# Kernel tuning notes

Measured on AMD Instinct MI355X. Metric: run time of the kernel, lower is better.

## Reference

```python
import jax, jax.numpy as jnp
import numpy as np

N_NODES = 100000


def gcn_conv(x, edge_index, W, b, n):
    """PyG-style GCNConv: h = D^-1/2 (A + I) D^-1/2 (x W) + b."""
    h = x @ W  # [n, out]
    loops = jnp.arange(n, dtype=edge_index.dtype)
    src = jnp.concatenate([edge_index[0], loops])
    dst = jnp.concatenate([edge_index[1], loops])
    deg = jax.ops.segment_sum(jnp.ones_like(dst, dtype=h.dtype), dst, num_segments=n)
    dinv = jnp.where(deg > 0, jax.lax.rsqrt(deg), 0.0)
    norm = dinv[src] * dinv[dst]  # [E+n]
    msg = h[src] * norm[:, None]
    out = jax.ops.segment_sum(msg, dst, num_segments=n)
    return out + b


def setup_inputs() -> dict:
    key = jax.random.key(0)
    ks = jax.random.split(key, 12)
    n, f, hid, c, e = N_NODES, 128, 16, 32, 3200000
    x = jax.random.normal(ks[0], (n, f), dtype=jnp.float32)
    edge_index_pos = jax.random.randint(ks[1], (2, e), 0, n, dtype=jnp.int32)
    edge_index_neg = jax.random.randint(ks[2], (2, e), 0, n, dtype=jnp.int32)
    def glorot(k, fi, fo):
        lim = np.sqrt(6.0 / (fi + fo)).astype(np.float32)
        return jax.random.uniform(k, (fi, fo), minval=-lim, maxval=lim, dtype=jnp.float32)
    return {
        "x": x,
        "edge_index_pos": edge_index_pos,
        "edge_index_neg": edge_index_neg,
        "W1p": glorot(ks[3], f, hid), "b1p": jnp.zeros((hid,), jnp.float32),
        "W1n": glorot(ks[4], f, hid), "b1n": jnp.zeros((hid,), jnp.float32),
        "W2p": glorot(ks[5], hid, c), "b2p": jnp.zeros((c,), jnp.float32),
        "W2n": glorot(ks[6], hid, c), "b2n": jnp.zeros((c,), jnp.float32),
    }


def reference(x, edge_index_pos, edge_index_neg, W1p, b1p, W1n, b1n, W2p, b2p, W2n, b2n):
    n = x.shape[0]
    # layer 1: relu(pos) - relu(neg)
    h = (jax.nn.relu(gcn_conv(x, edge_index_pos, W1p, b1p, n))
         - jax.nn.relu(gcn_conv(x, edge_index_neg, W1n, b1n, n)))
    # dropout is identity in eval mode (training=False)
    h = (jax.nn.relu(gcn_conv(h, edge_index_pos, W2p, b2p, n))
         - jax.nn.relu(gcn_conv(h, edge_index_neg, W2n, b2n, n)))
    return jax.nn.log_softmax(h, axis=1)
```

## Files before the change

### kernel.cpp

```cpp
#include <hip/hip_runtime.h>
#include <hip/hip_fp16.h>


#define BSHIFT 8
#define BSZ 256
#define MAX_NBK 512
#define FILL_CAP 13056
#define SORT_CAP 12032

__device__ __forceinline__ int chunk_of_block(int bid, int NCH) {
  return (NCH % 8 == 0) ? (bid % 8) * (NCH / 8) + bid / 8 : bid;
}


__global__ __launch_bounds__(256) void bucket_count2(
    const int* __restrict__ eP, const int* __restrict__ eN,
    int E, int CH, int NCH, int NBK, int* __restrict__ ccP, int* __restrict__ ccN) {
  __shared__ int cnt[MAX_NBK];
  const int* dsts = (blockIdx.y ? eN : eP) + E;
  int* cc = blockIdx.y ? ccN : ccP;
  const int c = chunk_of_block(blockIdx.x, NCH);
  for (int i = threadIdx.x; i < NBK; i += 256) cnt[i] = 0;
  __syncthreads();
  int base = c * CH, end = min(E, base + CH);
  for (int idx = base + threadIdx.x; idx < end; idx += 256)
    atomicAdd(&cnt[dsts[idx] >> BSHIFT], 1);
  __syncthreads();
  for (int i = threadIdx.x; i < NBK; i += 256)
    cc[(size_t)c * NBK + i] = cnt[i];
}

__global__ __launch_bounds__(512) void col_scan2(
    int* __restrict__ ccP, int* __restrict__ ccN, int NCH, int NBK,
    int* __restrict__ totP, int* __restrict__ totN) {
  __shared__ int s[512];
  int* cc = blockIdx.y ? ccN : ccP;
  int* tot = blockIdx.y ? totN : totP;
  int b = blockIdx.x, t = threadIdx.x;
  int v = (t < NCH) ? cc[(size_t)t * NBK + b] : 0;
  s[t] = v;
  for (int off = 1; off < 512; off <<= 1) {
    __syncthreads();
    int a = (t >= off) ? s[t - off] : 0;
    __syncthreads();
    s[t] += a;
  }
  __syncthreads();
  if (t < NCH) cc[(size_t)t * NBK + b] = s[t] - v;
  if (t == 511) tot[b] = s[511];
}

__global__ __launch_bounds__(512) void base_scan(
    const int* __restrict__ totP, const int* __restrict__ totN, int NBK,
    int* __restrict__ baseP, int* __restrict__ baseN,
    int* __restrict__ rowP, int* __restrict__ rowN, int n, int E) {
  __shared__ int sp[512], sn[512];
  __shared__ int carryP, carryN;
  int t = threadIdx.x;
  if (t == 0) { carryP = 0; carryN = 0; }
  __syncthreads();
  for (int tile = 0; tile < NBK; tile += 512) {
    int idx = tile + t;
    int vp = (idx < NBK) ? totP[idx] : 0;
    int vn = (idx < NBK) ? totN[idx] : 0;
    sp[t] = vp; sn[t] = vn;
    for (int off = 1; off < 512; off <<= 1) {
      __syncthreads();
      int ap = (t >= off) ? sp[t - off] : 0;
      int an = (t >= off) ? sn[t - off] : 0;
      __syncthreads();
      sp[t] += ap; sn[t] += an;
    }
    __syncthreads();
    if (idx < NBK) {
      baseP[idx] = carryP + sp[t] - vp;
      baseN[idx] = carryN + sn[t] - vn;
    }
    __syncthreads();
    if (t == 0) { carryP += sp[511]; carryN += sn[511]; }
    __syncthreads();
  }
  if (t == 0) {
    baseP[NBK] = E; baseN[NBK] = E;
    rowP[n] = E; rowN[n] = E;
  }
}

__global__ __launch_bounds__(512) void bucket_fill3(
    const int* __restrict__ eP, const int* __restrict__ eN,
    int E, int CH, int NCH, int NBK,
    const int* __restrict__ ccP, const int* __restrict__ ccN,
    const int* __restrict__ totP, const int* __restrict__ totN,
    const int* __restrict__ basP, const int* __restrict__ basN,
    unsigned* __restrict__ prP, unsigned* __restrict__ prN) {
  __shared__ unsigned obuf[FILL_CAP];
  __shared__ int chofs[MAX_NBK], hist[MAX_NBK], lofs[MAX_NBK], cur[MAX_NBK];
  __shared__ int s[512];
  const int* edges = blockIdx.y ? eN : eP;
  const int* cc = blockIdx.y ? ccN : ccP;
  const int* tot = blockIdx.y ? totN : totP;
  const int* bas = blockIdx.y ? basN : basP;
  unsigned* pairs = blockIdx.y ? prN : prP;
  const int c = chunk_of_block(blockIdx.x, NCH);
  const int t = threadIdx.x;

  int h = 0;
  if (t < NBK) {
    int o0 = cc[(size_t)c * NBK + t];
    int o1 = (c + 1 < NCH) ? cc[(size_t)(c + 1) * NBK + t] : tot[t];
    chofs[t] = o0;
    h = o1 - o0;
    hist[t] = h;
  }
  s[t] = h;
  for (int off = 1; off < 512; off <<= 1) {
    __syncthreads();
    int a = (t >= off) ? s[t - off] : 0;
    __syncthreads();
    s[t] += a;
  }
  __syncthreads();
  if (t < NBK) { lofs[t] = s[t] - hist[t]; cur[t] = s[t] - hist[t]; }
  __syncthreads();

  int base = c * CH, end = min(E, base + CH);
  for (int idx = base + t; idx < end; idx += 512) {
    int sv = edges[idx], d = edges[E + idx];
    int b = d >> BSHIFT;
    int pos = atomicAdd(&cur[b], 1);
    obuf[pos] = (unsigned)sv | ((unsigned)(d & (BSZ - 1)) << 24);
  }
  __syncthreads();

  if (t < NBK) {
    int cnt = hist[t], lo = lofs[t];
    unsigned* dst = pairs + (size_t)bas[t] + chofs[t];
    for (int j = 0; j < cnt; ++j) dst[j] = obuf[lo + j];
  }
}

__global__ __launch_bounds__(256) void tile_sort3(
    const unsigned* __restrict__ prP, const unsigned* __restrict__ prN,
    const int* __restrict__ basP, const int* __restrict__ basN, int n,
    float* __restrict__ dinvP, float* __restrict__ dinvN,
    int* __restrict__ rowP, int* __restrict__ rowN,
    unsigned* __restrict__ srcsP, unsigned* __restrict__ srcsN) {
  __shared__ unsigned obuf[SORT_CAP];
  __shared__ int hist[BSZ];
  __shared__ int scn[BSZ];
  __shared__ int cur[BSZ];
  const unsigned* pairs = blockIdx.y ? prN : prP;
  const int* base = blockIdx.y ? basN : basP;
  float* dinv = blockIdx.y ? dinvN : dinvP;
  int* rowoff = blockIdx.y ? rowN : rowP;
  unsigned* srcs = blockIdx.y ? srcsN : srcsP;
  const int b = blockIdx.x, t = threadIdx.x;
  const int s0 = base[b], s1 = base[b + 1], cnt = s1 - s0;
  hist[t] = 0;
  __syncthreads();
  for (int i = s0 + t; i < s1; i += 256)
    atomicAdd(&hist[pairs[i] >> 24], 1);
  __syncthreads();
  scn[t] = hist[t];
  __syncthreads();
  for (int off = 1; off < BSZ; off <<= 1) {
    int v = (t >= off) ? scn[t - off] : 0;
    __syncthreads();
    scn[t] += v;
    __syncthreads();
  }
  {
    int excl = scn[t] - hist[t];
    cur[t] = excl;
    int node = b * BSZ + t;
    if (node < n) {
      rowoff[node] = s0 + excl;
      dinv[node] = rsqrtf(1.0f + (float)hist[t]);
    }
  }
  __syncthreads();
  if (cnt <= SORT_CAP) {
    for (int i = s0 + t; i < s1; i += 256) {
      unsigned p = pairs[i];
      int pos = atomicAdd(&cur[p >> 24], 1);
      obuf[pos] = p & 0xFFFFFFu;
    }
    __syncthreads();
    for (int i = t; i < cnt; i += 256) srcs[s0 + i] = obuf[i];
  } else {
    for (int i = s0 + t; i < s1; i += 256) {
      unsigned p = pairs[i];
      int pos = atomicAdd(&cur[p >> 24], 1);
      srcs[s0 + pos] = p & 0xFFFFFFu;
    }
  }
}

__global__ __launch_bounds__(256) void xw1_kernel(
    const float* __restrict__ x, const float* __restrict__ Wp, const float* __restrict__ Wn,
    const float* __restrict__ dinvP, const float* __restrict__ dinvN,
    __half* __restrict__ hp, __half* __restrict__ hn, int n)
{
  __shared__ float xs[16 * 132];
  __shared__ float wp[128 * 16], wn[128 * 16];
  const int tid = threadIdx.x;
  const int rowBase = blockIdx.x * 16;

  for (int idx = tid; idx < 512; idx += 256) {
    ((float4*)wp)[idx] = ((const float4*)Wp)[idx];
    ((float4*)wn)[idx] = ((const float4*)Wn)[idx];
  }
  const int nrows = min(16, n - rowBase);
  for (int idx = tid; idx < nrows * 32; idx += 256) {
    int r = idx >> 5, c4 = idx & 31;
    float4 v = ((const float4*)(x + (size_t)(rowBase + r) * 128))[c4];
    *(float4*)(xs + r * 132 + c4 * 4) = v;
  }
  __syncthreads();

  const int r = tid >> 4, c = tid & 15;
  const int i = rowBase + r;
  if (i < n) {
    float ap = 0.f, an = 0.f;
    #pragma unroll
    for (int k = 0; k < 128; ++k) {
      float xv = xs[r * 132 + k];
      ap += xv * wp[k * 16 + c];
      an += xv * wn[k * 16 + c];
    }
    hp[(size_t)i * 16 + c] = __float2half(ap * dinvP[i]);
    hn[(size_t)i * 16 + c] = __float2half(an * dinvN[i]);
  }
}

__device__ __forceinline__ void fma_mix2(float& aLo, float& aHi, unsigned h2, float one) {
  asm("v_fma_mix_f32 %0, %2, %3, %0 op_sel:[0,0,0] op_sel_hi:[1,0,0]\n\t"
      "v_fma_mix_f32 %1, %2, %3, %1 op_sel:[1,0,0] op_sel_hi:[1,0,0]"
      : "+v"(aLo), "+v"(aHi)
      : "v"(h2), "v"(one));
}

__device__ __forceinline__ void seg_sum4(
    const unsigned* __restrict__ srcs, int e, int e1,
    const __half* __restrict__ tab, int lane4, float one,
    float& f0, float& f1, float& f2, float& f3)
{
  float g0 = 0.f, g1 = 0.f, g2 = 0.f, g3 = 0.f;
  for (; e + 8 <= e1; e += 8) {
    unsigned a[8];
    #pragma unroll
    for (int j = 0; j < 8; ++j) a[j] = srcs[e + j];
    uint2 v[8];
    #pragma unroll
    for (int j = 0; j < 8; ++j)
      v[j] = *(const uint2*)(tab + (size_t)a[j] * 16 + lane4 * 4);
    #pragma unroll
    for (int j = 0; j < 8; j += 2) {
      fma_mix2(f0, f1, v[j].x, one);
      fma_mix2(f2, f3, v[j].y, one);
      fma_mix2(g0, g1, v[j + 1].x, one);
      fma_mix2(g2, g3, v[j + 1].y, one);
    }
  }
  for (; e + 2 <= e1; e += 2) {
    unsigned a0 = srcs[e], a1 = srcs[e + 1];
    uint2 v0 = *(const uint2*)(tab + (size_t)a0 * 16 + lane4 * 4);
    uint2 v1 = *(const uint2*)(tab + (size_t)a1 * 16 + lane4 * 4);
    fma_mix2(f0, f1, v0.x, one);
    fma_mix2(f2, f3, v0.y, one);
    fma_mix2(g0, g1, v1.x, one);
    fma_mix2(g2, g3, v1.y, one);
  }
  if (e < e1) {
    uint2 v = *(const uint2*)(tab + (size_t)srcs[e] * 16 + lane4 * 4);
    fma_mix2(f0, f1, v.x, one);
    fma_mix2(f2, f3, v.y, one);
  }
  f0 += g0; f1 += g1; f2 += g2; f3 += g3;
}

__global__ __launch_bounds__(256) void agg_split(
    const unsigned* __restrict__ srcP, const int* __restrict__ rowP,
    const unsigned* __restrict__ srcN, const int* __restrict__ rowN,
    const __half* __restrict__ inP, const __half* __restrict__ inN,
    const float* __restrict__ dinvP, const float* __restrict__ dinvN,
    float* __restrict__ tmpP, float* __restrict__ tmpN, int n)
{
  const int gb = blockIdx.x;
  const int xcd = gb & 7;
  const int sign = xcd >> 2;
  const int nblk = (gb >> 3) * 4 + (xcd & 3);
  const int lane4 = threadIdx.x & 3, grp = threadIdx.x >> 2;
  const int i = nblk * 64 + grp;
  if (i >= n) return;

  const unsigned* srcs = sign ? srcN : srcP;
  const int* row = sign ? rowN : rowP;
  const __half* tab = sign ? inN : inP;
  const float* dinv = sign ? dinvN : dinvP;
  float* tmp = sign ? tmpN : tmpP;

  const float one = 1.0f;
  float f0 = 0.f, f1 = 0.f, f2 = 0.f, f3 = 0.f;
  uint2 self = *(const uint2*)(tab + (size_t)i * 16 + lane4 * 4);
  fma_mix2(f0, f1, self.x, one);
  fma_mix2(f2, f3, self.y, one);
  seg_sum4(srcs, row[i], row[i + 1], tab, lane4, one, f0, f1, f2, f3);
  const float d = dinv[i];
  float4 o;
  o.x = f0 * d; o.y = f1 * d; o.z = f2 * d; o.w = f3 * d;
  *(float4*)(tmp + (size_t)i * 16 + lane4 * 4) = o;
}

__global__ __launch_bounds__(256) void combine1(
    const float* __restrict__ tmpP, const float* __restrict__ tmpN,
    const float* __restrict__ bp, const float* __restrict__ bn,
    const float* __restrict__ dinvP, const float* __restrict__ dinvN,
    __half* __restrict__ Gp, __half* __restrict__ Gn, long long total)
{
  long long j = (long long)blockIdx.x * 256 + threadIdx.x;
  if (j >= total) return;
  int i = (int)(j >> 4), lane = (int)(j & 15);
  float ap = bp[lane] + tmpP[j];
  float an = bn[lane] + tmpN[j];
  float h = fmaxf(ap, 0.f) - fmaxf(an, 0.f);
  Gp[j] = __float2half(h * dinvP[i]);
  Gn[j] = __float2half(h * dinvN[i]);
}

__global__ __launch_bounds__(256) void final2(
    const float* __restrict__ Up, const float* __restrict__ Un,
    const float* __restrict__ W2p, const float* __restrict__ W2n,
    const float* __restrict__ b2p, const float* __restrict__ b2n,
    float* __restrict__ out, int n)
{
  __shared__ float wp[16 * 32], wn[16 * 32];
  for (int i = threadIdx.x; i < 512; i += 256) { wp[i] = W2p[i]; wn[i] = W2n[i]; }
  __syncthreads();

  const int tid = threadIdx.x;
  const int lane = tid & 15, grp = tid >> 4;
  const int i = blockIdx.x * 16 + grp;
  if (i >= n) return;

  float tp = Up[(size_t)i * 16 + lane];
  float tn = Un[(size_t)i * 16 + lane];

  float ap0 = b2p[lane], ap1 = b2p[lane + 16];
  float an0 = b2n[lane], an1 = b2n[lane + 16];
  #pragma unroll
  for (int k = 0; k < 16; ++k) {
    float tpk = __shfl(tp, k, 16);
    float tnk = __shfl(tn, k, 16);
    ap0 += tpk * wp[k * 32 + lane];
    ap1 += tpk * wp[k * 32 + lane + 16];
    an0 += tnk * wn[k * 32 + lane];
    an1 += tnk * wn[k * 32 + lane + 16];
  }
  float v0 = fmaxf(ap0, 0.f) - fmaxf(an0, 0.f);
  float v1 = fmaxf(ap1, 0.f) - fmaxf(an1, 0.f);
  float m = fmaxf(v0, v1);
  #pragma unroll
  for (int off = 8; off > 0; off >>= 1) m = fmaxf(m, __shfl_xor(m, off, 16));
  float s = __expf(v0 - m) + __expf(v1 - m);
  #pragma unroll
  for (int off = 8; off > 0; off >>= 1) s += __shfl_xor(s, off, 16);
  float ls = __logf(s);
  out[(size_t)i * 32 + lane] = v0 - m - ls;
  out[(size_t)i * 32 + lane + 16] = v1 - m - ls;
}

extern "C" void kernel_launch(void* const* d_in, const int* in_sizes, int n_in,
                              void* d_out, int out_size, void* d_ws, size_t ws_size,
                              hipStream_t stream) {
  const float* x   = (const float*)d_in[0];
  const int*   eP  = (const int*)d_in[1];
  const int*   eN  = (const int*)d_in[2];
  const float* W1p = (const float*)d_in[3];
  const float* b1p = (const float*)d_in[4];
  const float* W1n = (const float*)d_in[5];
  const float* b1n = (const float*)d_in[6];
  const float* W2p = (const float*)d_in[7];
  const float* b2p = (const float*)d_in[8];
  const float* W2n = (const float*)d_in[9];
  const float* b2n = (const float*)d_in[10];
  float* out = (float*)d_out;

  const int HID = in_sizes[4];
  const int F   = in_sizes[3] / HID;
  const int n   = in_sizes[0] / F;
  const int E   = in_sizes[1] / 2;
  (void)out_size; (void)n_in; (void)ws_size;

  const int NBK = (n + BSZ - 1) >> BSHIFT;
  const int CH  = (((E + 255) / 256) + 255) & ~255;
  const int NCH = (E + CH - 1) / CH;

  char* p = (char*)d_ws;
  auto alloc = [&](size_t bytes) { char* r = p; p += (bytes + 255) & ~(size_t)255; return r; };

  int*      ccP   = (int*)alloc((size_t)NCH * NBK * 4);
  int*      ccN   = (int*)alloc((size_t)NCH * NBK * 4);
  int*      totP  = (int*)alloc((size_t)NBK * 4);
  int*      totN  = (int*)alloc((size_t)NBK * 4);
  int*      basP  = (int*)alloc((size_t)(NBK + 1) * 4);
  int*      basN  = (int*)alloc((size_t)(NBK + 1) * 4);
  unsigned* prP   = (unsigned*)alloc((size_t)E * 4);
  unsigned* prN   = (unsigned*)alloc((size_t)E * 4);
  unsigned* srcP  = (unsigned*)alloc((size_t)E * 4);
  unsigned* srcN  = (unsigned*)alloc((size_t)E * 4);
  int*      rowP  = (int*)alloc((size_t)(n + 1) * 4);
  int*      rowN  = (int*)alloc((size_t)(n + 1) * 4);
  float*    dinvP = (float*)alloc((size_t)n * 4);
  float*    dinvN = (float*)alloc((size_t)n * 4);
  __half*   hsP   = (__half*)alloc((size_t)n * 16 * 2);
  __half*   hsN   = (__half*)alloc((size_t)n * 16 * 2);
  __half*   Gp    = (__half*)alloc((size_t)n * 16 * 2);
  __half*   Gn    = (__half*)alloc((size_t)n * 16 * 2);
  float*    tmpP  = (float*)alloc((size_t)n * 16 * 4);
  float*    tmpN  = (float*)alloc((size_t)n * 16 * 4);

  hipLaunchKernelGGL(bucket_count2, dim3(NCH, 2), dim3(256), 0, stream,
                     eP, eN, E, CH, NCH, NBK, ccP, ccN);
  hipLaunchKernelGGL(col_scan2, dim3(NBK, 2), dim3(512), 0, stream,
                     ccP, ccN, NCH, NBK, totP, totN);
  hipLaunchKernelGGL(base_scan, dim3(1), dim3(512), 0, stream,
                     totP, totN, NBK, basP, basN, rowP, rowN, n, E);
  hipLaunchKernelGGL(bucket_fill3, dim3(NCH, 2), dim3(512), 0, stream,
                     eP, eN, E, CH, NCH, NBK, ccP, ccN, totP, totN,
                     basP, basN, prP, prN);
  hipLaunchKernelGGL(tile_sort3, dim3(NBK, 2), dim3(256), 0, stream,
                     prP, prN, basP, basN, n, dinvP, dinvN, rowP, rowN, srcP, srcN);

  const int NB16 = (n + 15) / 16;
  const int NB64 = (n + 63) / 64;
  const int NBS  = ((NB64 + 3) / 4) * 4;
  const int GRID = NBS * 2;

  hipLaunchKernelGGL(xw1_kernel, dim3(NB16), dim3(256), 0, stream,
                     x, W1p, W1n, dinvP, dinvN, hsP, hsN, n);
  hipLaunchKernelGGL(agg_split, dim3(GRID), dim3(256), 0, stream,
                     srcP, rowP, srcN, rowN, hsP, hsN, dinvP, dinvN, tmpP, tmpN, n);
  hipLaunchKernelGGL(combine1, dim3((int)(((long long)n * 16 + 255) / 256)), dim3(256), 0, stream,
                     tmpP, tmpN, b1p, b1n, dinvP, dinvN, Gp, Gn, (long long)n * 16);

  hipLaunchKernelGGL(agg_split, dim3(GRID), dim3(256), 0, stream,
                     srcP, rowP, srcN, rowN, Gp, Gn, dinvP, dinvN, tmpP, tmpN, n);
  hipLaunchKernelGGL(final2, dim3(NB16), dim3(256), 0, stream,
                     tmpP, tmpN, W2p, W2n, b2p, b2n, out, n);
}
```

Baseline: 241.1 us.

## Use persistent work-stealing aggregation with XCC-aware sign selection and vectorized loads

The aggregation kernel becomes persistent: a fixed grid of blocks claims 64-node tiles through atomic counters. Each block first drains the sign (pos or neg) chosen from its hardware XCC ID, then the other sign. The edge loop reads 16 source indices per uint4 batch after aligning the start to a multiple of 4, and launch bounds request higher occupancy. Separately, bucket_fill copies each bucket with a whole wavefront instead of one thread, and combine1 processes four elements per thread with vector loads and stores. The aim is better load balance on skewed degrees and fewer memory transactions, at the cost of atomic contention, extra barriers and counters that base_scan must reset.

```diff
diff --git a/kernel.cpp b/kernel.cpp
--- a/kernel.cpp
+++ b/kernel.cpp
@@ -53,7 +53,8 @@
 __global__ __launch_bounds__(512) void base_scan(
     const int* __restrict__ totP, const int* __restrict__ totN, int NBK,
     int* __restrict__ baseP, int* __restrict__ baseN,
-    int* __restrict__ rowP, int* __restrict__ rowN, int n, int E) {
+    int* __restrict__ rowP, int* __restrict__ rowN, int n, int E,
+    int* __restrict__ aggc) {
   __shared__ int sp[512], sn[512];
   __shared__ int carryP, carryN;
   int t = threadIdx.x;
@@ -83,6 +84,7 @@
   if (t == 0) {
     baseP[NBK] = E; baseN[NBK] = E;
     rowP[n] = E; rowN[n] = E;
+    aggc[0] = 0; aggc[1] = 0; aggc[2] = 0; aggc[3] = 0;
   }
 }
 
@@ -132,10 +134,11 @@
   }
   __syncthreads();
 
-  if (t < NBK) {
-    int cnt = hist[t], lo = lofs[t];
-    unsigned* dst = pairs + (size_t)bas[t] + chofs[t];
-    for (int j = 0; j < cnt; ++j) dst[j] = obuf[lo + j];
+  const int wv = t >> 6, ln = t & 63;
+  for (int b = wv; b < NBK; b += 8) {
+    int cnt2 = hist[b], lo = lofs[b];
+    unsigned* dst = pairs + (size_t)bas[b] + chofs[b];
+    for (int j = ln; j < cnt2; j += 64) dst[j] = obuf[lo + j];
   }
 }
 
@@ -240,92 +243,129 @@
       : "v"(h2), "v"(one));
 }
 
-__device__ __forceinline__ void seg_sum4(
-    const unsigned* __restrict__ srcs, int e, int e1,
-    const __half* __restrict__ tab, int lane4, float one,
-    float& f0, float& f1, float& f2, float& f3)
-{
-  float g0 = 0.f, g1 = 0.f, g2 = 0.f, g3 = 0.f;
-  for (; e + 8 <= e1; e += 8) {
-    unsigned a[8];
-    #pragma unroll
-    for (int j = 0; j < 8; ++j) a[j] = srcs[e + j];
-    uint2 v[8];
-    #pragma unroll
-    for (int j = 0; j < 8; ++j)
-      v[j] = *(const uint2*)(tab + (size_t)a[j] * 16 + lane4 * 4);
-    #pragma unroll
-    for (int j = 0; j < 8; j += 2) {
-      fma_mix2(f0, f1, v[j].x, one);
-      fma_mix2(f2, f3, v[j].y, one);
-      fma_mix2(g0, g1, v[j + 1].x, one);
-      fma_mix2(g2, g3, v[j + 1].y, one);
-    }
-  }
-  for (; e + 2 <= e1; e += 2) {
-    unsigned a0 = srcs[e], a1 = srcs[e + 1];
-    uint2 v0 = *(const uint2*)(tab + (size_t)a0 * 16 + lane4 * 4);
-    uint2 v1 = *(const uint2*)(tab + (size_t)a1 * 16 + lane4 * 4);
-    fma_mix2(f0, f1, v0.x, one);
-    fma_mix2(f2, f3, v0.y, one);
-    fma_mix2(g0, g1, v1.x, one);
-    fma_mix2(g2, g3, v1.y, one);
-  }
-  if (e < e1) {
-    uint2 v = *(const uint2*)(tab + (size_t)srcs[e] * 16 + lane4 * 4);
-    fma_mix2(f0, f1, v.x, one);
-    fma_mix2(f2, f3, v.y, one);
-  }
-  f0 += g0; f1 += g1; f2 += g2; f3 += g3;
-}
-
-__global__ __launch_bounds__(256) void agg_split(
+__global__ __launch_bounds__(256, 6) void agg_split(
     const unsigned* __restrict__ srcP, const int* __restrict__ rowP,
     const unsigned* __restrict__ srcN, const int* __restrict__ rowN,
     const __half* __restrict__ inP, const __half* __restrict__ inN,
     const float* __restrict__ dinvP, const float* __restrict__ dinvN,
-    float* __restrict__ tmpP, float* __restrict__ tmpN, int n)
+    float* __restrict__ tmpP, float* __restrict__ tmpN,
+    int n, int NBU, int* __restrict__ ctr)
 {
-  const int gb = blockIdx.x;
-  const int xcd = gb & 7;
-  const int sign = xcd >> 2;
-  const int nblk = (gb >> 3) * 4 + (xcd & 3);
+  __shared__ int sh_t;
+  unsigned xcc;
+  asm("s_getreg_b32 %0, hwreg(HW_REG_XCC_ID)" : "=s"(xcc));
+  int s = (int)((xcc & 7u) >> 2);
   const int lane4 = threadIdx.x & 3, grp = threadIdx.x >> 2;
-  const int i = nblk * 64 + grp;
-  if (i >= n) return;
-
-  const unsigned* srcs = sign ? srcN : srcP;
-  const int* row = sign ? rowN : rowP;
-  const __half* tab = sign ? inN : inP;
-  const float* dinv = sign ? dinvN : dinvP;
-  float* tmp = sign ? tmpN : tmpP;
-
   const float one = 1.0f;
-  float f0 = 0.f, f1 = 0.f, f2 = 0.f, f3 = 0.f;
-  uint2 self = *(const uint2*)(tab + (size_t)i * 16 + lane4 * 4);
-  fma_mix2(f0, f1, self.x, one);
-  fma_mix2(f2, f3, self.y, one);
-  seg_sum4(srcs, row[i], row[i + 1], tab, lane4, one, f0, f1, f2, f3);
-  const float d = dinv[i];
-  float4 o;
-  o.x = f0 * d; o.y = f1 * d; o.z = f2 * d; o.w = f3 * d;
-  *(float4*)(tmp + (size_t)i * 16 + lane4 * 4) = o;
+
+  for (int pass = 0; pass < 2; ++pass, s ^= 1) {
+    const unsigned* __restrict__ srcs = s ? srcN : srcP;
+    const int* __restrict__ row = s ? rowN : rowP;
+    const __half* __restrict__ tab = s ? inN : inP;
+    const float* __restrict__ dinv = s ? dinvN : dinvP;
+    float* __restrict__ tmp = s ? tmpN : tmpP;
+    int* c = ctr + s;
+
+    if (threadIdx.x == 0) sh_t = atomicAdd(c, 1);
+    __syncthreads();
+    int t = sh_t;
+    while (t < NBU) {
+      __syncthreads();
+      if (threadIdx.x == 0) sh_t = atomicAdd(c, 1);
+
+      const int i = t * 64 + grp;
+      if (i < n) {
+        int e = row[i], e1 = row[i + 1];
+        float f0 = 0.f, f1 = 0.f, f2 = 0.f, f3 = 0.f;
+        float g0 = 0.f, g1 = 0.f, g2 = 0.f, g3 = 0.f;
+        {
+          uint2 v = *(const uint2*)(tab + (size_t)i * 16 + lane4 * 4);
+          fma_mix2(f0, f1, v.x, one);
+          fma_mix2(f2, f3, v.y, one);
+        }
+        while (e < e1 && (e & 3)) {
+          uint2 v = *(const uint2*)(tab + (size_t)srcs[e] * 16 + lane4 * 4);
+          fma_mix2(g0, g1, v.x, one);
+          fma_mix2(g2, g3, v.y, one);
+          ++e;
+        }
+        for (; e + 16 <= e1; e += 16) {
+          uint4 ia = *(const uint4*)(srcs + e);
+          uint4 ib = *(const uint4*)(srcs + e + 4);
+          uint4 ic = *(const uint4*)(srcs + e + 8);
+          uint4 id = *(const uint4*)(srcs + e + 12);
+          unsigned idx[16] = {ia.x, ia.y, ia.z, ia.w, ib.x, ib.y, ib.z, ib.w,
+                              ic.x, ic.y, ic.z, ic.w, id.x, id.y, id.z, id.w};
+          uint2 v[16];
+          #pragma unroll
+          for (int j = 0; j < 16; ++j)
+            v[j] = *(const uint2*)(tab + (size_t)idx[j] * 16 + lane4 * 4);
+          #pragma unroll
+          for (int j = 0; j < 16; j += 2) {
+            fma_mix2(f0, f1, v[j].x, one);
+            fma_mix2(f2, f3, v[j].y, one);
+            fma_mix2(g0, g1, v[j + 1].x, one);
+            fma_mix2(g2, g3, v[j + 1].y, one);
+          }
+        }
+        for (; e + 4 <= e1; e += 4) {
+          uint4 ia = *(const uint4*)(srcs + e);
+          uint2 v0 = *(const uint2*)(tab + (size_t)ia.x * 16 + lane4 * 4);
+          uint2 v1 = *(const uint2*)(tab + (size_t)ia.y * 16 + lane4 * 4);
+          uint2 v2 = *(const uint2*)(tab + (size_t)ia.z * 16 + lane4 * 4);
+          uint2 v3 = *(const uint2*)(tab + (size_t)ia.w * 16 + lane4 * 4);
+          fma_mix2(f0, f1, v0.x, one);
+          fma_mix2(f2, f3, v0.y, one);
+          fma_mix2(g0, g1, v1.x, one);
+          fma_mix2(g2, g3, v1.y, one);
+          fma_mix2(f0, f1, v2.x, one);
+          fma_mix2(f2, f3, v2.y, one);
+          fma_mix2(g0, g1, v3.x, one);
+          fma_mix2(g2, g3, v3.y, one);
+        }
+        for (; e < e1; ++e) {
+          uint2 v = *(const uint2*)(tab + (size_t)srcs[e] * 16 + lane4 * 4);
+          fma_mix2(f0, f1, v.x, one);
+          fma_mix2(f2, f3, v.y, one);
+        }
+        const float d = dinv[i];
+        float4 o;
+        o.x = (f0 + g0) * d; o.y = (f1 + g1) * d;
+        o.z = (f2 + g2) * d; o.w = (f3 + g3) * d;
+        *(float4*)(tmp + (size_t)i * 16 + lane4 * 4) = o;
+      }
+      __syncthreads();
+      t = sh_t;
+    }
+    __syncthreads();
+  }
 }
 
 __global__ __launch_bounds__(256) void combine1(
     const float* __restrict__ tmpP, const float* __restrict__ tmpN,
     const float* __restrict__ bp, const float* __restrict__ bn,
     const float* __restrict__ dinvP, const float* __restrict__ dinvN,
-    __half* __restrict__ Gp, __half* __restrict__ Gn, long long total)
+    __half* __restrict__ Gp, __half* __restrict__ Gn, int nq)
 {
-  long long j = (long long)blockIdx.x * 256 + threadIdx.x;
-  if (j >= total) return;
-  int i = (int)(j >> 4), lane = (int)(j & 15);
-  float ap = bp[lane] + tmpP[j];
-  float an = bn[lane] + tmpN[j];
-  float h = fmaxf(ap, 0.f) - fmaxf(an, 0.f);
-  Gp[j] = __float2half(h * dinvP[i]);
-  Gn[j] = __float2half(h * dinvN[i]);
+  int q = blockIdx.x * 256 + threadIdx.x;
+  if (q >= nq) return;
+  int i = q >> 2;
+  float4 tp = ((const float4*)tmpP)[q];
+  float4 tn = ((const float4*)tmpN)[q];
+  float4 bpv = ((const float4*)bp)[q & 3];
+  float4 bnv = ((const float4*)bn)[q & 3];
+  float dp = dinvP[i], dn = dinvN[i];
+  float h0 = fmaxf(bpv.x + tp.x, 0.f) - fmaxf(bnv.x + tn.x, 0.f);
+  float h1 = fmaxf(bpv.y + tp.y, 0.f) - fmaxf(bnv.y + tn.y, 0.f);
+  float h2 = fmaxf(bpv.z + tp.z, 0.f) - fmaxf(bnv.z + tn.z, 0.f);
+  float h3 = fmaxf(bpv.w + tp.w, 0.f) - fmaxf(bnv.w + tn.w, 0.f);
+  union { uint2 u; __half2 h[2]; } a, b;
+  a.h[0] = __floats2half2_rn(h0 * dp, h1 * dp);
+  a.h[1] = __floats2half2_rn(h2 * dp, h3 * dp);
+  b.h[0] = __floats2half2_rn(h0 * dn, h1 * dn);
+  b.h[1] = __floats2half2_rn(h2 * dn, h3 * dn);
+  ((uint2*)Gp)[q] = a.u;
+  ((uint2*)Gn)[q] = b.u;
 }
 
 __global__ __launch_bounds__(256) void final2(
@@ -419,13 +459,14 @@
   __half*   Gn    = (__half*)alloc((size_t)n * 16 * 2);
   float*    tmpP  = (float*)alloc((size_t)n * 16 * 4);
   float*    tmpN  = (float*)alloc((size_t)n * 16 * 4);
+  int*      aggc  = (int*)alloc(4 * sizeof(int));
 
   hipLaunchKernelGGL(bucket_count2, dim3(NCH, 2), dim3(256), 0, stream,
                      eP, eN, E, CH, NCH, NBK, ccP, ccN);
   hipLaunchKernelGGL(col_scan2, dim3(NBK, 2), dim3(512), 0, stream,
                      ccP, ccN, NCH, NBK, totP, totN);
   hipLaunchKernelGGL(base_scan, dim3(1), dim3(512), 0, stream,
-                     totP, totN, NBK, basP, basN, rowP, rowN, n, E);
+                     totP, totN, NBK, basP, basN, rowP, rowN, n, E, aggc);
   hipLaunchKernelGGL(bucket_fill3, dim3(NCH, 2), dim3(512), 0, stream,
                      eP, eN, E, CH, NCH, NBK, ccP, ccN, totP, totN,
                      basP, basN, prP, prN);
@@ -433,19 +474,20 @@
                      prP, prN, basP, basN, n, dinvP, dinvN, rowP, rowN, srcP, srcN);
 
   const int NB16 = (n + 15) / 16;
-  const int NB64 = (n + 63) / 64;
-  const int NBS  = ((NB64 + 3) / 4) * 4;
-  const int GRID = NBS * 2;
+  const int NBU  = (n + 63) / 64;
+  const int AGGB = 4096;
 
   hipLaunchKernelGGL(xw1_kernel, dim3(NB16), dim3(256), 0, stream,
                      x, W1p, W1n, dinvP, dinvN, hsP, hsN, n);
-  hipLaunchKernelGGL(agg_split, dim3(GRID), dim3(256), 0, stream,
-                     srcP, rowP, srcN, rowN, hsP, hsN, dinvP, dinvN, tmpP, tmpN, n);
-  hipLaunchKernelGGL(combine1, dim3((int)(((long long)n * 16 + 255) / 256)), dim3(256), 0, stream,
-                     tmpP, tmpN, b1p, b1n, dinvP, dinvN, Gp, Gn, (long long)n * 16);
-
-  hipLaunchKernelGGL(agg_split, dim3(GRID), dim3(256), 0, stream,
-                     srcP, rowP, srcN, rowN, Gp, Gn, dinvP, dinvN, tmpP, tmpN, n);
+  hipLaunchKernelGGL(agg_split, dim3(AGGB), dim3(256), 0, stream,
+                     srcP, rowP, srcN, rowN, hsP, hsN, dinvP, dinvN, tmpP, tmpN,
+                     n, NBU, aggc + 0);
+  hipLaunchKernelGGL(combine1, dim3((n * 4 + 255) / 256), dim3(256), 0, stream,
+                     tmpP, tmpN, b1p, b1n, dinvP, dinvN, Gp, Gn, n * 4);
+
+  hipLaunchKernelGGL(agg_split, dim3(AGGB), dim3(256), 0, stream,
+                     srcP, rowP, srcN, rowN, Gp, Gn, dinvP, dinvN, tmpP, tmpN,
+                     n, NBU, aggc + 2);
   hipLaunchKernelGGL(final2, dim3(NB16), dim3(256), 0, stream,
                      tmpP, tmpN, W2p, W2n, b2p, b2n, out, n);
 }
```

After: 454.3 us. +88.4%, slower.
